# Performance work log

Hardware: AMD Instinct MI355X
Metric: run time of the kernel (lower is better)

Reference implementation:

```python
import jax, jax.numpy as jnp
import numpy as np

N_NODES = 50000
N_EDGES = 800000
IN_DIM = 128
HID_DIM = 128
BN_EPS = 1e-5


def setup_inputs() -> dict:
    key = jax.random.key(0)
    ks = jax.random.split(key, 16)
    s = 0.02
    inp = {
        "h": jax.random.normal(ks[0], (N_NODES, IN_DIM), jnp.float32),
        "x": jax.random.normal(ks[1], (N_NODES, 3), jnp.float32),
        "e": jax.random.randint(ks[2], (2, N_EDGES), 0, N_NODES, jnp.int32),
        # BatchNorm affine params
        "bn_gamma": jnp.ones((IN_DIM,), jnp.float32),
        "bn_beta": jnp.zeros((IN_DIM,), jnp.float32),
        # f_e: Linear(2*in+1 -> hid), SiLU, Linear(hid -> hid), SiLU
        "fe_w1": jax.random.normal(ks[3], (HID_DIM, 2 * IN_DIM + 1), jnp.float32) * s,
        "fe_b1": jnp.zeros((HID_DIM,), jnp.float32),
        "fe_w2": jax.random.normal(ks[4], (HID_DIM, HID_DIM), jnp.float32) * s,
        "fe_b2": jnp.zeros((HID_DIM,), jnp.float32),
        # f_inf: Linear(hid -> 1), Sigmoid
        "finf_w": jax.random.normal(ks[5], (1, HID_DIM), jnp.float32) * s,
        "finf_b": jnp.zeros((1,), jnp.float32),
        # f_h: Linear(in+hid -> hid), SiLU, Linear(hid -> hid)
        "fh_w1": jax.random.normal(ks[6], (HID_DIM, IN_DIM + HID_DIM), jnp.float32) * s,
        "fh_b1": jnp.zeros((HID_DIM,), jnp.float32),
        "fh_w2": jax.random.normal(ks[7], (HID_DIM, HID_DIM), jnp.float32) * s,
        "fh_b2": jnp.zeros((HID_DIM,), jnp.float32),
    }
    return inp


def reference(h, x, e, bn_gamma, bn_beta, fe_w1, fe_b1, fe_w2, fe_b2,
              finf_w, finf_b, fh_w1, fh_b1, fh_w2, fh_b2):
    # BatchNorm1d (training-mode batch stats, biased variance)
    mean = jnp.mean(h, axis=0)
    var = jnp.var(h, axis=0)
    h = (h - mean) * jax.lax.rsqrt(var + BN_EPS) * bn_gamma + bn_beta

    e_st, e_end = e[0], e[1]
    # pairwise distances per edge: [E, 1]
    diff = x[e_st] - x[e_end]
    dists = jnp.sqrt(jnp.sum(diff * diff, axis=1, keepdims=True))

    # edge message MLP f_e on [E, 2*in+1]
    tmp = jnp.concatenate([h[e_st], h[e_end], dists], axis=1)
    m_ij = jax.nn.silu(tmp @ fe_w1.T + fe_b1)
    m_ij = jax.nn.silu(m_ij @ fe_w2.T + fe_b2)

    # gate f_inf: [E, 1]
    e_ij = jax.nn.sigmoid(m_ij @ finf_w.T + finf_b)

    # gated scatter-sum aggregation over source index e[0]
    m_i = jax.ops.segment_sum(e_ij * m_ij, e_st, num_segments=h.shape[0])

    # node update f_h with residual
    u = jax.nn.silu(jnp.concatenate([h, m_i], axis=1) @ fh_w1.T + fh_b1)
    h = h + (u @ fh_w2.T + fh_b2)
    return (h, e)
```

## Files before the change

### kernel.cpp

```cpp
#include <hip/hip_runtime.h>
#include <math.h>

#define N_NODES 50000
#define N_EDGES 800000
#define DIM 128
#define EB 64
#define SCAN_B 196
#define BN_B 256
#define HIST_B 3125
#define ECOPY_B 1563
#define PREP_B 385
#define APPLY_B 6250
#define MIZ_B 6250

typedef __attribute__((ext_vector_type(8))) short short8v;
typedef __attribute__((ext_vector_type(4))) float f32x4;

__device__ __forceinline__ float silu_f(float v) { return __fdividef(v, 1.f + __expf(-v)); }

__device__ __forceinline__ unsigned short f2bf(float f) {
  unsigned u = __float_as_uint(f);
  return (unsigned short)((u + 0x7fffu + ((u >> 16) & 1u)) >> 16);
}

__global__ void k1_fused_kernel(const float* __restrict__ h, const int* __restrict__ e,
                                const float* __restrict__ fe_w1, const float* __restrict__ fe_w2,
                                const float* __restrict__ fh_w1, const float* __restrict__ fh_w2,
                                float* __restrict__ stats, int* __restrict__ cnt,
                                float* __restrict__ out_e, unsigned short* __restrict__ w1bf,
                                float* __restrict__ w1col, unsigned short* __restrict__ w2bf,
                                unsigned short* __restrict__ fw1bf, unsigned short* __restrict__ fw2bf) {
  __shared__ float red[256];
  const int bid = blockIdx.x;
  const int tid = threadIdx.x;

  if (bid < BN_B) {
    const int c = tid & 127;
    const int rs = tid >> 7;
    float s = 0.f, s2 = 0.f;
    for (int row = bid * 2 + rs; row < N_NODES; row += BN_B * 2) {
      float v = h[(size_t)row * DIM + c];
      s += v;
      s2 += v * v;
    }
    red[tid] = s;
    __syncthreads();
    if (tid < 128) atomicAdd(&stats[c], red[c] + red[c + 128]);
    __syncthreads();
    red[tid] = s2;
    __syncthreads();
    if (tid < 128) atomicAdd(&stats[DIM + c], red[c] + red[c + 128]);
    return;
  }
  if (bid < BN_B + HIST_B) {
    const int i = (bid - BN_B) * 256 + tid;
    if (i < N_EDGES) atomicAdd(&cnt[e[i]], 1);
    return;
  }
  if (bid < BN_B + HIST_B + ECOPY_B) {
    const int i4 = (bid - BN_B - HIST_B) * 256 + tid;
    if (i4 < 2 * N_EDGES / 4) {
      const int4 v = ((const int4*)e)[i4];
      float4 o;
      o.x = (float)v.x;
      o.y = (float)v.y;
      o.z = (float)v.z;
      o.w = (float)v.w;
      ((float4*)out_e)[i4] = o;
    }
    return;
  }
  int idx = (bid - BN_B - HIST_B - ECOPY_B) * 256 + tid;
  if (idx < 32768) {
    int o = idx >> 8, k = idx & 255;
    w1bf[idx] = f2bf(fe_w1[(size_t)o * 257 + k]);
    return;
  }
  idx -= 32768;
  if (idx < 128) { w1col[idx] = fe_w1[(size_t)idx * 257 + 256]; return; }
  idx -= 128;
  if (idx < 16384) { w2bf[idx] = f2bf(fe_w2[idx]); return; }
  idx -= 16384;
  if (idx < 32768) { fw1bf[idx] = f2bf(fh_w1[idx]); return; }
  idx -= 32768;
  if (idx < 16384) { fw2bf[idx] = f2bf(fh_w2[idx]); return; }
}

__global__ void k2_fused_kernel(const int* __restrict__ cnt, int* __restrict__ bsum,
                                float* __restrict__ stats, const float* __restrict__ gamma,
                                const float* __restrict__ beta) {
  __shared__ int red[256];
  const int bid = blockIdx.x;
  const int t = threadIdx.x;
  if (bid < SCAN_B) {
    const int i = bid * 256 + t;
    red[t] = (i < N_NODES) ? cnt[i] : 0;
    __syncthreads();
    for (int off = 128; off > 0; off >>= 1) {
      if (t < off) red[t] += red[t + off];
      __syncthreads();
    }
    if (t == 0) bsum[bid] = red[0];
    return;
  }
  if (t < 128) {
    const float inv_n = 1.f / (float)N_NODES;
    float mean = stats[t] * inv_n;
    float var = stats[DIM + t] * inv_n - mean * mean;
    float s = gamma[t] * rsqrtf(var + 1e-5f);
    stats[2 * DIM + t] = s;
    stats[3 * DIM + t] = beta[t] - mean * s;
  }
}

__global__ void scanB_kernel(int* __restrict__ bsum) {
  __shared__ int s[256];
  const int t = threadIdx.x;
  const int v = (t < SCAN_B) ? bsum[t] : 0;
  s[t] = v;
  __syncthreads();
  for (int off = 1; off < 256; off <<= 1) {
    const int add = (t >= off) ? s[t - off] : 0;
    __syncthreads();
    s[t] += add;
    __syncthreads();
  }
  if (t < SCAN_B) bsum[t] = s[t] - v;
}

__global__ void k3_fused_kernel(const int* __restrict__ cnt, const int* __restrict__ bsum,
                                int* __restrict__ cursor, const float* __restrict__ h,
                                const float* __restrict__ stats, unsigned short* __restrict__ hbf,
                                float* __restrict__ mi_g) {
  __shared__ int s[256];
  const int bid = blockIdx.x;
  const int t = threadIdx.x;
  if (bid < SCAN_B) {
    const int i = bid * 256 + t;
    const int v = (i < N_NODES) ? cnt[i] : 0;
    s[t] = v;
    __syncthreads();
    for (int off = 1; off < 256; off <<= 1) {
      const int add = (t >= off) ? s[t - off] : 0;
      __syncthreads();
      s[t] += add;
      __syncthreads();
    }
    if (i < N_NODES) cursor[i] = bsum[bid] + s[t] - v;
    return;
  }
  if (bid < SCAN_B + APPLY_B) {
    const int i4 = (bid - SCAN_B) * 256 + t;
    const int c4 = i4 & 31;
    const float4 v = ((const float4*)h)[i4];
    const float4 a = ((const float4*)(stats + 2 * DIM))[c4];
    const float4 b = ((const float4*)(stats + 3 * DIM))[c4];
    ushort4 o;
    o.x = f2bf(v.x * a.x + b.x);
    o.y = f2bf(v.y * a.y + b.y);
    o.z = f2bf(v.z * a.z + b.z);
    o.w = f2bf(v.w * a.w + b.w);
    ((ushort4*)hbf)[i4] = o;
    return;
  }
  const int i4 = (bid - SCAN_B - APPLY_B) * 256 + t;
  ((float4*)mi_g)[i4] = (float4){0.f, 0.f, 0.f, 0.f};
}

__global__ void sort_scatter_kernel(const int* __restrict__ e, const float* __restrict__ x,
                                    int* __restrict__ cursor, int* __restrict__ srcS,
                                    int* __restrict__ dstS, float* __restrict__ distS) {
  const int i = blockIdx.x * blockDim.x + threadIdx.x;
  if (i >= N_EDGES) return;
  const int s = e[i], d = e[N_EDGES + i];
  const float dx = x[s * 3 + 0] - x[d * 3 + 0];
  const float dy = x[s * 3 + 1] - x[d * 3 + 1];
  const float dz = x[s * 3 + 2] - x[d * 3 + 2];
  const int pos = atomicAdd(&cursor[s], 1);
  srcS[pos] = s;
  dstS[pos] = d;
  distS[pos] = sqrtf(dx * dx + dy * dy + dz * dz);
}

__launch_bounds__(256, 6)
__global__ void edge_mfma_kernel(const unsigned short* __restrict__ hbf,
                                 const int* __restrict__ srcS, const int* __restrict__ dstS,
                                 const float* __restrict__ distS,
                                 const unsigned short* __restrict__ w1bf, const float* __restrict__ w1col,
                                 const float* __restrict__ b1, const unsigned short* __restrict__ w2bf,
                                 const float* __restrict__ b2, const float* __restrict__ winf,
                                 const float* __restrict__ binf, float* __restrict__ mi_g) {
  __shared__ unsigned short buf[EB * 128];
  __shared__ int srcs[EB];
  __shared__ int dsts[EB];
  __shared__ float dists[EB];
  __shared__ float gbuf[EB][5];
  __shared__ float gate[EB];

  const int tid = threadIdx.x;
  const int l = tid & 63, w = tid >> 6;
  const int r16 = l & 15, g = l >> 4;
  const int ebase = blockIdx.x * EB;

  if (tid < EB) {
    srcs[tid] = srcS[ebase + tid];
    dsts[tid] = dstS[ebase + tid];
    dists[tid] = distS[ebase + tid];
  }
  __syncthreads();

  const int er_s = tid >> 2, cb_s = (tid & 3) * 4;

  {
    const unsigned short* ps = hbf + (size_t)srcs[er_s] * DIM;
#pragma unroll
    for (int j = 0; j < 4; ++j) {
      const int c = cb_s + j;
      *(int4*)&buf[er_s * 128 + ((c ^ (er_s & 7)) << 3)] = *(const int4*)(ps + c * 8);
    }
  }
  __syncthreads();

  f32x4 acc[4][2];
#pragma unroll
  for (int m_ = 0; m_ < 4; ++m_)
#pragma unroll
    for (int ni = 0; ni < 2; ++ni) acc[m_][ni] = (f32x4){0.f, 0.f, 0.f, 0.f};

#pragma unroll
  for (int kb = 0; kb < 4; ++kb) {
    short8v a[4], b[2];
#pragma unroll
    for (int m_ = 0; m_ < 4; ++m_) {
      const int er = m_ * 16 + r16;
      a[m_] = *(const short8v*)&buf[er * 128 + (((kb * 4 + g) ^ (er & 7)) << 3)];
    }
#pragma unroll
    for (int ni = 0; ni < 2; ++ni) {
      const int o = w * 32 + ni * 16 + r16;
      b[ni] = *(const short8v*)&w1bf[o * 256 + kb * 32 + g * 8];
    }
#pragma unroll
    for (int m_ = 0; m_ < 4; ++m_)
#pragma unroll
      for (int ni = 0; ni < 2; ++ni)
        acc[m_][ni] = __builtin_amdgcn_mfma_f32_16x16x32_bf16(a[m_], b[ni], acc[m_][ni], 0, 0, 0);
  }
  __syncthreads();

  {
    const unsigned short* pd = hbf + (size_t)dsts[er_s] * DIM;
#pragma unroll
    for (int j = 0; j < 4; ++j) {
      const int c = cb_s + j;
      *(int4*)&buf[er_s * 128 + ((c ^ (er_s & 7)) << 3)] = *(const int4*)(pd + c * 8);
    }
  }
  __syncthreads();

#pragma unroll
  for (int kb = 4; kb < 8; ++kb) {
    short8v a[4], b[2];
#pragma unroll
    for (int m_ = 0; m_ < 4; ++m_) {
      const int er = m_ * 16 + r16;
      a[m_] = *(const short8v*)&buf[er * 128 + ((((kb - 4) * 4 + g) ^ (er & 7)) << 3)];
    }
#pragma unroll
    for (int ni = 0; ni < 2; ++ni) {
      const int o = w * 32 + ni * 16 + r16;
      b[ni] = *(const short8v*)&w1bf[o * 256 + kb * 32 + g * 8];
    }
#pragma unroll
    for (int m_ = 0; m_ < 4; ++m_)
#pragma unroll
      for (int ni = 0; ni < 2; ++ni)
        acc[m_][ni] = __builtin_amdgcn_mfma_f32_16x16x32_bf16(a[m_], b[ni], acc[m_][ni], 0, 0, 0);
  }
  __syncthreads();

  {
    const int o0 = w * 32 + r16, o1 = o0 + 16;
    const float wc0 = w1col[o0], wc1 = w1col[o1];
    const float bb0 = b1[o0], bb1 = b1[o1];
#pragma unroll
    for (int m_ = 0; m_ < 4; ++m_)
#pragma unroll
      for (int r = 0; r < 4; ++r) {
        const int er = m_ * 16 + g * 4 + r;
        const float dd = dists[er];
        buf[er * 128 + (o0 ^ ((er & 7) << 3))] = f2bf(silu_f(acc[m_][0][r] + dd * wc0 + bb0));
        buf[er * 128 + (o1 ^ ((er & 7) << 3))] = f2bf(silu_f(acc[m_][1][r] + dd * wc1 + bb1));
      }
  }
  __syncthreads();

  f32x4 acc2[4][2];
#pragma unroll
  for (int m_ = 0; m_ < 4; ++m_)
#pragma unroll
    for (int ni = 0; ni < 2; ++ni) acc2[m_][ni] = (f32x4){0.f, 0.f, 0.f, 0.f};

#pragma unroll
  for (int kb = 0; kb < 4; ++kb) {
    short8v a[4], b[2];
    const int k0 = kb * 32 + g * 8;
#pragma unroll
    for (int m_ = 0; m_ < 4; ++m_) {
      const int er = m_ * 16 + r16;
      a[m_] = *(const short8v*)&buf[er * 128 + (k0 ^ ((er & 7) << 3))];
    }
#pragma unroll
    for (int ni = 0; ni < 2; ++ni) {
      const int o = w * 32 + ni * 16 + r16;
      b[ni] = *(const short8v*)&w2bf[o * 128 + k0];
    }
#pragma unroll
    for (int m_ = 0; m_ < 4; ++m_)
#pragma unroll
      for (int ni = 0; ni < 2; ++ni)
        acc2[m_][ni] = __builtin_amdgcn_mfma_f32_16x16x32_bf16(a[m_], b[ni], acc2[m_][ni], 0, 0, 0);
  }

  float pv[16];
  {
    const int o0 = w * 32 + r16, o1 = o0 + 16;
    const float b20 = b2[o0], b21 = b2[o1];
    const float wf0 = winf[o0], wf1 = winf[o1];
#pragma unroll
    for (int m_ = 0; m_ < 4; ++m_)
#pragma unroll
      for (int r = 0; r < 4; ++r) {
        const float v0 = silu_f(acc2[m_][0][r] + b20);
        const float v1 = silu_f(acc2[m_][1][r] + b21);
        acc2[m_][0][r] = v0;
        acc2[m_][1][r] = v1;
        pv[m_ * 4 + r] = v0 * wf0 + v1 * wf1;
      }
  }

  {
    const bool s0 = r16 & 1;
#pragma unroll
    for (int j = 0; j < 8; ++j) {
      const float lo = pv[2 * j], hi = pv[2 * j + 1];
      const float other = __shfl_xor(s0 ? lo : hi, 1, 64);
      pv[j] = (s0 ? hi : lo) + other;
    }
    const bool s1 = r16 & 2;
#pragma unroll
    for (int j = 0; j < 4; ++j) {
      const float lo = pv[2 * j], hi = pv[2 * j + 1];
      const float other = __shfl_xor(s1 ? lo : hi, 2, 64);
      pv[j] = (s1 ? hi : lo) + other;
    }
    const bool s2 = r16 & 4;
#pragma unroll
    for (int j = 0; j < 2; ++j) {
      const float lo = pv[2 * j], hi = pv[2 * j + 1];
      const float other = __shfl_xor(s2 ? lo : hi, 4, 64);
      pv[j] = (s2 ? hi : lo) + other;
    }
    const bool s3 = r16 & 8;
    {
      const float lo = pv[0], hi = pv[1];
      const float other = __shfl_xor(s3 ? lo : hi, 8, 64);
      pv[0] = (s3 ? hi : lo) + other;
    }
    const int er = (r16 >> 2) * 16 + g * 4 + (r16 & 3);
    gbuf[er][w] = pv[0];
  }
  __syncthreads();
  if (tid < EB) {
    const float s = gbuf[tid][0] + gbuf[tid][1] + gbuf[tid][2] + gbuf[tid][3] + binf[0];
    gate[tid] = __fdividef(1.f, 1.f + __expf(-s));
  }
  __syncthreads();

  {
    const int o0 = w * 32 + r16, o1 = o0 + 16;
#pragma unroll
    for (int m_ = 0; m_ < 4; ++m_)
#pragma unroll
      for (int r = 0; r < 4; ++r) {
        const int er = m_ * 16 + g * 4 + r;
        const float gg = gate[er];
        buf[er * 128 + (o0 ^ ((er & 7) << 3))] = f2bf(acc2[m_][0][r] * gg);
        buf[er * 128 + (o1 ^ ((er & 7) << 3))] = f2bf(acc2[m_][1][r] * gg);
      }
  }
  __syncthreads();

  {
    const int c = tid & 127;
    const int r0 = (tid >> 7) * 32;
    int cur = srcs[r0];
    float a = 0.f;
    for (int row = r0; row < r0 + 32; ++row) {
      const int s = srcs[row];
      if (s != cur) {
        atomicAdd(&mi_g[(size_t)cur * DIM + c], a);
        a = 0.f;
        cur = s;
      }
      a += __uint_as_float((unsigned)buf[row * 128 + (c ^ ((row & 7) << 3))] << 16);
    }
    atomicAdd(&mi_g[(size_t)cur * DIM + c], a);
  }
}

__launch_bounds__(256, 6)
__global__ void node_mfma_kernel(const unsigned short* __restrict__ hbf,
                                 const float* __restrict__ mi_g,
                                 const float* __restrict__ h, const float* __restrict__ stats,
                                 const unsigned short* __restrict__ fw1, const float* __restrict__ fb1,
                                 const unsigned short* __restrict__ fw2, const float* __restrict__ fb2,
                                 float* __restrict__ out) {
  __shared__ unsigned short buf[EB * 128];

  const int tid = threadIdx.x;
  const int l = tid & 63, w = tid >> 6;
  const int r16 = l & 15, g = l >> 4;
  const int nbase = blockIdx.x * EB;

  const int er_s = tid >> 2, cb_s = (tid & 3) * 4;
  int nstg = nbase + er_s;
  if (nstg >= N_NODES) nstg = N_NODES - 1;

  {
    const unsigned short* ps = hbf + (size_t)nstg * DIM;
#pragma unroll
    for (int j = 0; j < 4; ++j) {
      const int c = cb_s + j;
      *(int4*)&buf[er_s * 128 + ((c ^ (er_s & 7)) << 3)] = *(const int4*)(ps + c * 8);
    }
  }
  __syncthreads();

  f32x4 acc[4][2];
#pragma unroll
  for (int m_ = 0; m_ < 4; ++m_)
#pragma unroll
    for (int ni = 0; ni < 2; ++ni) acc[m_][ni] = (f32x4){0.f, 0.f, 0.f, 0.f};

#pragma unroll
  for (int kb = 0; kb < 4; ++kb) {
    short8v a[4], b[2];
#pragma unroll
    for (int m_ = 0; m_ < 4; ++m_) {
      const int er = m_ * 16 + r16;
      a[m_] = *(const short8v*)&buf[er * 128 + (((kb * 4 + g) ^ (er & 7)) << 3)];
    }
#pragma unroll
    for (int ni = 0; ni < 2; ++ni) {
      const int o = w * 32 + ni * 16 + r16;
      b[ni] = *(const short8v*)&fw1[o * 256 + kb * 32 + g * 8];
    }
#pragma unroll
    for (int m_ = 0; m_ < 4; ++m_)
#pragma unroll
      for (int ni = 0; ni < 2; ++ni)
        acc[m_][ni] = __builtin_amdgcn_mfma_f32_16x16x32_bf16(a[m_], b[ni], acc[m_][ni], 0, 0, 0);
  }
  __syncthreads();

  {
    const float* pm = mi_g + (size_t)nstg * DIM;
#pragma unroll
    for (int j = 0; j < 4; ++j) {
      const int c = cb_s + j;
      const float4 f0 = *(const float4*)(pm + c * 8);
      const float4 f1 = *(const float4*)(pm + c * 8 + 4);
      int4 v;
      v.x = (int)f2bf(f0.x) | ((int)f2bf(f0.y) << 16);
      v.y = (int)f2bf(f0.z) | ((int)f2bf(f0.w) << 16);
      v.z = (int)f2bf(f1.x) | ((int)f2bf(f1.y) << 16);
      v.w = (int)f2bf(f1.z) | ((int)f2bf(f1.w) << 16);
      *(int4*)&buf[er_s * 128 + ((c ^ (er_s & 7)) << 3)] = v;
    }
  }
  __syncthreads();

#pragma unroll
  for (int kb = 4; kb < 8; ++kb) {
    short8v a[4], b[2];
#pragma unroll
    for (int m_ = 0; m_ < 4; ++m_) {
      const int er = m_ * 16 + r16;
      a[m_] = *(const short8v*)&buf[er * 128 + ((((kb - 4) * 4 + g) ^ (er & 7)) << 3)];
    }
#pragma unroll
    for (int ni = 0; ni < 2; ++ni) {
      const int o = w * 32 + ni * 16 + r16;
      b[ni] = *(const short8v*)&fw1[o * 256 + kb * 32 + g * 8];
    }
#pragma unroll
    for (int m_ = 0; m_ < 4; ++m_)
#pragma unroll
      for (int ni = 0; ni < 2; ++ni)
        acc[m_][ni] = __builtin_amdgcn_mfma_f32_16x16x32_bf16(a[m_], b[ni], acc[m_][ni], 0, 0, 0);
  }
  __syncthreads();

  {
    const int o0 = w * 32 + r16, o1 = o0 + 16;
    const float bb0 = fb1[o0], bb1 = fb1[o1];
#pragma unroll
    for (int m_ = 0; m_ < 4; ++m_)
#pragma unroll
      for (int r = 0; r < 4; ++r) {
        const int er = m_ * 16 + g * 4 + r;
        buf[er * 128 + (o0 ^ ((er & 7) << 3))] = f2bf(silu_f(acc[m_][0][r] + bb0));
        buf[er * 128 + (o1 ^ ((er & 7) << 3))] = f2bf(silu_f(acc[m_][1][r] + bb1));
      }
  }
  __syncthreads();

  f32x4 acc2[4][2];
#pragma unroll
  for (int m_ = 0; m_ < 4; ++m_)
#pragma unroll
    for (int ni = 0; ni < 2; ++ni) acc2[m_][ni] = (f32x4){0.f, 0.f, 0.f, 0.f};

#pragma unroll
  for (int kb = 0; kb < 4; ++kb) {
    short8v a[4], b[2];
    const int k0 = kb * 32 + g * 8;
#pragma unroll
    for (int m_ = 0; m_ < 4; ++m_) {
      const int er = m_ * 16 + r16;
      a[m_] = *(const short8v*)&buf[er * 128 + (k0 ^ ((er & 7) << 3))];
    }
#pragma unroll
    for (int ni = 0; ni < 2; ++ni) {
      const int o = w * 32 + ni * 16 + r16;
      b[ni] = *(const short8v*)&fw2[o * 128 + k0];
    }
#pragma unroll
    for (int m_ = 0; m_ < 4; ++m_)
#pragma unroll
      for (int ni = 0; ni < 2; ++ni)
        acc2[m_][ni] = __builtin_amdgcn_mfma_f32_16x16x32_bf16(a[m_], b[ni], acc2[m_][ni], 0, 0, 0);
  }

#pragma unroll
  for (int ni = 0; ni < 2; ++ni) {
    const int o = w * 32 + ni * 16 + r16;
    const float bb = fb2[o];
    const float sc = stats[2 * DIM + o];
    const float sh = stats[3 * DIM + o];
#pragma unroll
    for (int m_ = 0; m_ < 4; ++m_)
#pragma unroll
      for (int r = 0; r < 4; ++r) {
        const int n = nbase + m_ * 16 + g * 4 + r;
        if (n < N_NODES) {
          const float hv = h[(size_t)n * DIM + o];
          out[(size_t)n * DIM + o] = hv * sc + sh + acc2[m_][ni][r] + bb;
        }
      }
  }
}

extern "C" void kernel_launch(void* const* d_in, const int* in_sizes, int n_in, void* d_out,
                              int out_size, void* d_ws, size_t ws_size, hipStream_t stream) {
  const float* h = (const float*)d_in[0];
  const float* x = (const float*)d_in[1];
  const int* e = (const int*)d_in[2];
  const float* bn_gamma = (const float*)d_in[3];
  const float* bn_beta = (const float*)d_in[4];
  const float* fe_w1 = (const float*)d_in[5];
  const float* fe_b1 = (const float*)d_in[6];
  const float* fe_w2 = (const float*)d_in[7];
  const float* fe_b2 = (const float*)d_in[8];
  const float* finf_w = (const float*)d_in[9];
  const float* finf_b = (const float*)d_in[10];
  const float* fh_w1 = (const float*)d_in[11];
  const float* fh_b1 = (const float*)d_in[12];
  const float* fh_w2 = (const float*)d_in[13];
  const float* fh_b2 = (const float*)d_in[14];

  char* wp = (char*)d_ws;
  auto alloc = [&](size_t bytes) -> char* {
    char* p = wp;
    wp += (bytes + 255) & ~(size_t)255;
    return p;
  };
  float* stats = (float*)alloc(512 * sizeof(float));
  int* cnt = (int*)alloc((size_t)N_NODES * 4);
  unsigned short* hbf = (unsigned short*)alloc((size_t)N_NODES * DIM * 2);
  unsigned short* w1bf = (unsigned short*)alloc(128 * 256 * 2);
  float* w1col = (float*)alloc(128 * 4);
  unsigned short* w2bf = (unsigned short*)alloc(128 * 128 * 2);
  unsigned short* fw1bf = (unsigned short*)alloc(128 * 256 * 2);
  unsigned short* fw2bf = (unsigned short*)alloc(128 * 128 * 2);
  int* cursor = (int*)alloc((size_t)N_NODES * 4);
  int* bsum = (int*)alloc((size_t)SCAN_B * 4);
  int* srcS = (int*)alloc((size_t)N_EDGES * 4);
  int* dstS = (int*)alloc((size_t)N_EDGES * 4);
  float* distS = (float*)alloc((size_t)N_EDGES * 4);
  float* mi_g = (float*)alloc((size_t)N_NODES * DIM * 4);

  float* out = (float*)d_out;
  float* out_e = out + (size_t)N_NODES * DIM;

  hipMemsetAsync(stats, 0, 2048 + (size_t)N_NODES * 4, stream);

  k1_fused_kernel<<<BN_B + HIST_B + ECOPY_B + PREP_B, 256, 0, stream>>>(
      h, e, fe_w1, fe_w2, fh_w1, fh_w2, stats, cnt, out_e, w1bf, w1col, w2bf, fw1bf, fw2bf);
  k2_fused_kernel<<<SCAN_B + 1, 256, 0, stream>>>(cnt, bsum, stats, bn_gamma, bn_beta);
  scanB_kernel<<<1, 256, 0, stream>>>(bsum);
  k3_fused_kernel<<<SCAN_B + APPLY_B + MIZ_B, 256, 0, stream>>>(cnt, bsum, cursor, h, stats, hbf,
                                                                mi_g);
  sort_scatter_kernel<<<(N_EDGES + 255) / 256, 256, 0, stream>>>(e, x, cursor, srcS, dstS, distS);
  edge_mfma_kernel<<<N_EDGES / EB, 256, 0, stream>>>(hbf, srcS, dstS, distS, w1bf, w1col, fe_b1,
                                                     w2bf, fe_b2, finf_w, finf_b, mi_g);
  node_mfma_kernel<<<(N_NODES + EB - 1) / EB, 256, 0, stream>>>(hbf, mi_g, h, stats, fw1bf, fh_b1,
                                                                fw2bf, fh_b2, out);
}
```

Measured before the change: 532.2 us.

## Gather src and dst rows together, remap blocks per XCD, keep fp32 messages

The edge kernel now gathers both source and destination bf16 feature rows into a single 64x256 shared tile in one pass. This removes a barrier-separated second gather and allows one 8-step K loop for the first GEMM. Blocks are remapped so consecutive sorted-edge chunks run on the same XCD, which improves L2 locality for the segmented atomic adds. Gated messages are now kept in fp32 in shared memory instead of being rounded to bf16, and launch bounds drop from 6 to 4 waves per SIMD. The trade-off is doubled LDS per block and possibly lower occupancy.

```diff
diff --git a/kernel.cpp b/kernel.cpp
--- a/kernel.cpp
+++ b/kernel.cpp
@@ -182,7 +182,7 @@
   distS[pos] = sqrtf(dx * dx + dy * dy + dz * dz);
 }
 
-__launch_bounds__(256, 6)
+__launch_bounds__(256, 4)
 __global__ void edge_mfma_kernel(const unsigned short* __restrict__ hbf,
                                  const int* __restrict__ srcS, const int* __restrict__ dstS,
                                  const float* __restrict__ distS,
@@ -190,17 +190,26 @@
                                  const float* __restrict__ b1, const unsigned short* __restrict__ w2bf,
                                  const float* __restrict__ b2, const float* __restrict__ winf,
                                  const float* __restrict__ binf, float* __restrict__ mi_g) {
-  __shared__ unsigned short buf[EB * 128];
+  __shared__ unsigned short Abuf[EB * 256];
   __shared__ int srcs[EB];
   __shared__ int dsts[EB];
   __shared__ float dists[EB];
   __shared__ float gbuf[EB][5];
   __shared__ float gate[EB];
 
+  unsigned short* A2 = Abuf;
+  float* Mf = (float*)Abuf;
+
   const int tid = threadIdx.x;
   const int l = tid & 63, w = tid >> 6;
   const int r16 = l & 15, g = l >> 4;
-  const int ebase = blockIdx.x * EB;
+
+  const int nwg = N_EDGES / EB;
+  const int q = nwg >> 3, r = nwg & 7;
+  const int xcd = blockIdx.x & 7;
+  const int idx = blockIdx.x >> 3;
+  const int bid = (xcd < r ? xcd * (q + 1) : r * (q + 1) + (xcd - r) * q) + idx;
+  const int ebase = bid * EB;
 
   if (tid < EB) {
     srcs[tid] = srcS[ebase + tid];
@@ -209,14 +218,15 @@
   }
   __syncthreads();
 
-  const int er_s = tid >> 2, cb_s = (tid & 3) * 4;
-
-  {
-    const unsigned short* ps = hbf + (size_t)srcs[er_s] * DIM;
-#pragma unroll
-    for (int j = 0; j < 4; ++j) {
-      const int c = cb_s + j;
-      *(int4*)&buf[er_s * 128 + ((c ^ (er_s & 7)) << 3)] = *(const int4*)(ps + c * 8);
+  {
+    const int er = tid >> 2, cb = (tid & 3) * 8;
+    const unsigned short* ps = hbf + (size_t)srcs[er] * DIM;
+    const unsigned short* pd = hbf + (size_t)dsts[er] * DIM;
+#pragma unroll
+    for (int j = 0; j < 8; ++j) {
+      const int c = cb + j;
+      const int4 v = (c < 16) ? *(const int4*)(ps + c * 8) : *(const int4*)(pd + (c - 16) * 8);
+      *(int4*)&Abuf[er * 256 + ((c ^ (er & 7)) << 3)] = v;
     }
   }
   __syncthreads();
@@ -227,13 +237,13 @@
 #pragma unroll
     for (int ni = 0; ni < 2; ++ni) acc[m_][ni] = (f32x4){0.f, 0.f, 0.f, 0.f};
 
-#pragma unroll
-  for (int kb = 0; kb < 4; ++kb) {
+  for (int kb = 0; kb < 8; ++kb) {
     short8v a[4], b[2];
 #pragma unroll
     for (int m_ = 0; m_ < 4; ++m_) {
       const int er = m_ * 16 + r16;
-      a[m_] = *(const short8v*)&buf[er * 128 + (((kb * 4 + g) ^ (er & 7)) << 3)];
+      const int chunk = kb * 4 + g;
+      a[m_] = *(const short8v*)&Abuf[er * 256 + ((chunk ^ (er & 7)) << 3)];
     }
 #pragma unroll
     for (int ni = 0; ni < 2; ++ni) {
@@ -249,48 +259,19 @@
   __syncthreads();
 
   {
-    const unsigned short* pd = hbf + (size_t)dsts[er_s] * DIM;
-#pragma unroll
-    for (int j = 0; j < 4; ++j) {
-      const int c = cb_s + j;
-      *(int4*)&buf[er_s * 128 + ((c ^ (er_s & 7)) << 3)] = *(const int4*)(pd + c * 8);
-    }
-  }
-  __syncthreads();
-
-#pragma unroll
-  for (int kb = 4; kb < 8; ++kb) {
-    short8v a[4], b[2];
-#pragma unroll
-    for (int m_ = 0; m_ < 4; ++m_) {
-      const int er = m_ * 16 + r16;
-      a[m_] = *(const short8v*)&buf[er * 128 + ((((kb - 4) * 4 + g) ^ (er & 7)) << 3)];
-    }
-#pragma unroll
-    for (int ni = 0; ni < 2; ++ni) {
-      const int o = w * 32 + ni * 16 + r16;
-      b[ni] = *(const short8v*)&w1bf[o * 256 + kb * 32 + g * 8];
-    }
-#pragma unroll
-    for (int m_ = 0; m_ < 4; ++m_)
-#pragma unroll
-      for (int ni = 0; ni < 2; ++ni)
-        acc[m_][ni] = __builtin_amdgcn_mfma_f32_16x16x32_bf16(a[m_], b[ni], acc[m_][ni], 0, 0, 0);
-  }
-  __syncthreads();
-
-  {
     const int o0 = w * 32 + r16, o1 = o0 + 16;
     const float wc0 = w1col[o0], wc1 = w1col[o1];
     const float bb0 = b1[o0], bb1 = b1[o1];
 #pragma unroll
     for (int m_ = 0; m_ < 4; ++m_)
 #pragma unroll
-      for (int r = 0; r < 4; ++r) {
-        const int er = m_ * 16 + g * 4 + r;
+      for (int r_ = 0; r_ < 4; ++r_) {
+        const int er = m_ * 16 + g * 4 + r_;
         const float dd = dists[er];
-        buf[er * 128 + (o0 ^ ((er & 7) << 3))] = f2bf(silu_f(acc[m_][0][r] + dd * wc0 + bb0));
-        buf[er * 128 + (o1 ^ ((er & 7) << 3))] = f2bf(silu_f(acc[m_][1][r] + dd * wc1 + bb1));
+        const float v0 = silu_f(acc[m_][0][r_] + dd * wc0 + bb0);
+        const float v1 = silu_f(acc[m_][1][r_] + dd * wc1 + bb1);
+        A2[er * 128 + (o0 ^ ((er & 7) << 3))] = f2bf(v0);
+        A2[er * 128 + (o1 ^ ((er & 7) << 3))] = f2bf(v1);
       }
   }
   __syncthreads();
@@ -301,14 +282,13 @@
 #pragma unroll
     for (int ni = 0; ni < 2; ++ni) acc2[m_][ni] = (f32x4){0.f, 0.f, 0.f, 0.f};
 
-#pragma unroll
   for (int kb = 0; kb < 4; ++kb) {
     short8v a[4], b[2];
     const int k0 = kb * 32 + g * 8;
 #pragma unroll
     for (int m_ = 0; m_ < 4; ++m_) {
       const int er = m_ * 16 + r16;
-      a[m_] = *(const short8v*)&buf[er * 128 + (k0 ^ ((er & 7) << 3))];
+      a[m_] = *(const short8v*)&A2[er * 128 + (k0 ^ ((er & 7) << 3))];
     }
 #pragma unroll
     for (int ni = 0; ni < 2; ++ni) {
@@ -330,12 +310,12 @@
 #pragma unroll
     for (int m_ = 0; m_ < 4; ++m_)
 #pragma unroll
-      for (int r = 0; r < 4; ++r) {
-        const float v0 = silu_f(acc2[m_][0][r] + b20);
-        const float v1 = silu_f(acc2[m_][1][r] + b21);
-        acc2[m_][0][r] = v0;
-        acc2[m_][1][r] = v1;
-        pv[m_ * 4 + r] = v0 * wf0 + v1 * wf1;
+      for (int r_ = 0; r_ < 4; ++r_) {
+        const float v0 = silu_f(acc2[m_][0][r_] + b20);
+        const float v1 = silu_f(acc2[m_][1][r_] + b21);
+        acc2[m_][0][r_] = v0;
+        acc2[m_][1][r_] = v1;
+        pv[m_ * 4 + r_] = v0 * wf0 + v1 * wf1;
       }
   }
 
@@ -382,11 +362,11 @@
 #pragma unroll
     for (int m_ = 0; m_ < 4; ++m_)
 #pragma unroll
-      for (int r = 0; r < 4; ++r) {
-        const int er = m_ * 16 + g * 4 + r;
+      for (int r_ = 0; r_ < 4; ++r_) {
+        const int er = m_ * 16 + g * 4 + r_;
         const float gg = gate[er];
-        buf[er * 128 + (o0 ^ ((er & 7) << 3))] = f2bf(acc2[m_][0][r] * gg);
-        buf[er * 128 + (o1 ^ ((er & 7) << 3))] = f2bf(acc2[m_][1][r] * gg);
+        Mf[er * 128 + (o0 ^ ((er & 7) << 2))] = acc2[m_][0][r_] * gg;
+        Mf[er * 128 + (o1 ^ ((er & 7) << 2))] = acc2[m_][1][r_] * gg;
       }
   }
   __syncthreads();
@@ -403,7 +383,7 @@
         a = 0.f;
         cur = s;
       }
-      a += __uint_as_float((unsigned)buf[row * 128 + (c ^ ((row & 7) << 3))] << 16);
+      a += Mf[row * 128 + (c ^ ((row & 7) << 2))];
     }
     atomicAdd(&mi_g[(size_t)cur * DIM + c], a);
   }
@@ -508,10 +488,10 @@
 #pragma unroll
     for (int m_ = 0; m_ < 4; ++m_)
 #pragma unroll
-      for (int r = 0; r < 4; ++r) {
-        const int er = m_ * 16 + g * 4 + r;
-        buf[er * 128 + (o0 ^ ((er & 7) << 3))] = f2bf(silu_f(acc[m_][0][r] + bb0));
-        buf[er * 128 + (o1 ^ ((er & 7) << 3))] = f2bf(silu_f(acc[m_][1][r] + bb1));
+      for (int r_ = 0; r_ < 4; ++r_) {
+        const int er = m_ * 16 + g * 4 + r_;
+        buf[er * 128 + (o0 ^ ((er & 7) << 3))] = f2bf(silu_f(acc[m_][0][r_] + bb0));
+        buf[er * 128 + (o1 ^ ((er & 7) << 3))] = f2bf(silu_f(acc[m_][1][r_] + bb1));
       }
   }
   __syncthreads();
@@ -552,11 +532,11 @@
 #pragma unroll
     for (int m_ = 0; m_ < 4; ++m_)
 #pragma unroll
-      for (int r = 0; r < 4; ++r) {
-        const int n = nbase + m_ * 16 + g * 4 + r;
+      for (int r_ = 0; r_ < 4; ++r_) {
+        const int n = nbase + m_ * 16 + g * 4 + r_;
         if (n < N_NODES) {
           const float hv = h[(size_t)n * DIM + o];
-          out[(size_t)n * DIM + o] = hv * sc + sh + acc2[m_][ni][r] + bb;
+          out[(size_t)n * DIM + o] = hv * sc + sh + acc2[m_][ni][r_] + bb;
         }
       }
   }
```

New measurement: 478.5 us. 10.1% less time.
